# Performance work log

Measured on AMD Instinct MI355X. Metric: run time of the kernel, lower is better.

Reference implementation:

```python
import jax, jax.numpy as jnp
import numpy as np

N = 1024      # n_nodes
S = 32        # state_dim
M = 32        # message_dim
STEPS = 5     # n_steps


def setup_inputs() -> dict:
    key = jax.random.key(0)
    ks = jax.random.split(key, 12)
    w = lambda k, shape: jax.random.normal(k, shape, jnp.float32) * 0.02
    return {
        "J": jax.random.normal(ks[0], (N, N), jnp.float32),
        "b": jax.random.normal(ks[1], (N,), jnp.float32),
        # message_passing MLP (Linear(2S+3->M), Linear(M->M), Linear(M->M))
        "W1": w(ks[2], (M, 2 * S + 3)), "b1": jnp.zeros((M,), jnp.float32),
        "W2": w(ks[3], (M, M)),         "b2": jnp.zeros((M,), jnp.float32),
        "W3": w(ks[4], (M, M)),         "b3": jnp.zeros((M,), jnp.float32),
        # GRU(input=S+M, hidden=S). h0 is always zero in the original forward,
        # so weight_hh never contributes (only bias_hh does) and is omitted.
        "W_ih": w(ks[5], (3 * S, S + M)),
        "b_ih": w(ks[6], (3 * S,)),
        "b_hh": w(ks[7], (3 * S,)),
        # readout MLP (Linear(S->M), Linear(M->M), Linear(M->2))
        "R1": w(ks[8], (M, S)),  "rb1": jnp.zeros((M,), jnp.float32),
        "R2": w(ks[9], (M, M)),  "rb2": jnp.zeros((M,), jnp.float32),
        "R3": w(ks[10], (2, M)), "rb3": jnp.zeros((2,), jnp.float32),
    }


def reference(J, b, W1, b1, W2, b2, W3, b3, W_ih, b_ih, b_hh, R1, rb1, R2, rb2, R3, rb3):
    # Split first linear over the concat [h_i, h_j, J_ij, b_i, b_j] so the
    # [N, N, 2S+3] concat tensor is never materialized.
    W1a, W1b = W1[:, :S], W1[:, S:2 * S]
    wJ, wbi, wbj = W1[:, 2 * S], W1[:, 2 * S + 1], W1[:, 2 * S + 2]

    def step(h, _):
        hi = h @ W1a.T                       # [N, M] (sender part)
        hj = h @ W1b.T                       # [N, M] (receiver part)
        pre = (hi[:, None, :] + hj[None, :, :]
               + J[:, :, None] * wJ
               + b[:, None, None] * wbi
               + b[None, :, None] * wbj
               + b1)                          # [N, N, M]
        x = jax.nn.relu(pre)
        x = jax.nn.relu(x @ W2.T + b2)
        x = jax.nn.relu(x @ W3.T + b3)       # message_i_j: [N, N, M]
        m = x.sum(0)                          # message to node j: sum over senders i
        # GRU with zero initial hidden state: h' = (1-z) * n_gate
        gi = jnp.concatenate([h, m], axis=-1) @ W_ih.T + b_ih  # [N, 3S]
        r = jax.nn.sigmoid(gi[:, :S] + b_hh[:S])
        z = jax.nn.sigmoid(gi[:, S:2 * S] + b_hh[S:2 * S])
        n = jnp.tanh(gi[:, 2 * S:] + r * b_hh[2 * S:])
        return (1.0 - z) * n, None

    h0 = jnp.zeros((N, S), J.dtype)
    h, _ = jax.lax.scan(step, h0, None, length=STEPS)

    r = jax.nn.relu(h @ R1.T + rb1)
    r = jax.nn.relu(r @ R2.T + rb2)
    r = jax.nn.relu(r @ R3.T + rb3)          # [N, 2]
    return jax.nn.sigmoid(r)
```

## Files before the change

kernel.cpp:

```cpp
#include <hip/hip_runtime.h>
#include <math.h>

#define NN 1024

typedef __attribute__((ext_vector_type(8))) short bf16x8;
typedef __attribute__((ext_vector_type(4))) float f32x4;
typedef __attribute__((ext_vector_type(2))) float f32x2;
typedef __attribute__((ext_vector_type(4))) unsigned int u32x4;

__device__ __forceinline__ float sigmoidf_(float x) { return 1.0f / (1.0f + __expf(-x)); }

__device__ __forceinline__ unsigned int pk2(float a, float b) {
    return __builtin_amdgcn_perm(__float_as_uint(a) + 0x8000u,
                                 __float_as_uint(b) + 0x8000u, 0x03020706u);
}
__device__ __forceinline__ unsigned int pkcvt(float a, float b) {
#if __has_builtin(__builtin_amdgcn_cvt_pk_bf16_f32)
    return __builtin_bit_cast(unsigned int, __builtin_amdgcn_cvt_pk_bf16_f32(a, b));
#else
    return pk2(a, b);
#endif
}
__device__ __forceinline__ unsigned short f2bf_rne(float a) {
    unsigned int ua = __float_as_uint(a);
    ua += 0x7fffu + ((ua >> 16) & 1u);
    return (unsigned short)(ua >> 16);
}

#define CFG_FLOATS 2560

__global__ __launch_bounds__(256) void k_pre(
    const float* __restrict__ J, const float* __restrict__ b,
    const float* __restrict__ W1, const float* __restrict__ b1,
    const float* __restrict__ W2, const float* __restrict__ b2,
    const float* __restrict__ W3, const float* __restrict__ b3,
    float* __restrict__ Jt, float* __restrict__ h,
    float* __restrict__ u0, float* __restrict__ v, float* __restrict__ cfg)
{
    __shared__ float tile[32][33];
    const int t = blockIdx.x;
    const int tid = threadIdx.x;
    if (t < 1024) {
        int tx = (t & 31) * 32, ty = (t >> 5) * 32;
        int x = tid & 31, y = tid >> 5;
#pragma unroll
        for (int r = 0; r < 4; r++)
            tile[y + 8 * r][x] = J[(size_t)(ty + y + 8 * r) * NN + tx + x];
        __syncthreads();
#pragma unroll
        for (int r = 0; r < 4; r++)
            Jt[(size_t)(tx + y + 8 * r) * NN + ty + x] = tile[x][y + 8 * r];
    } else if (t < 1152) {
        int idx = (t - 1024) * 256 + tid;
        int row = idx >> 5, mm = idx & 31;
        float bi = b[row];
        h[idx]  = 0.f;
        u0[idx] = bi * W1[mm * 67 + 65];
        v[idx]  = fmaf(bi, W1[mm * 67 + 66], b1[mm]);
    } else if (tid < 64) {
        const int l = tid, p = l & 15, q = l >> 4;
        union FU { unsigned int d[4]; unsigned short s[8]; } t0, t1, t2, t3;
        float wj[8];
#pragma unroll
        for (int jj = 0; jj < 8; jj++) {
            int k = q * 8 + jj;
            t0.s[jj] = f2bf_rne(W2[p * 32 + k]);
            t1.s[jj] = f2bf_rne(W2[(16 + p) * 32 + k]);
            t2.s[jj] = f2bf_rne(W3[p * 32 + k]);
            t3.s[jj] = f2bf_rne(W3[(16 + p) * 32 + k]);
            wj[jj] = W1[k * 67 + 64];
        }
        u32x4* cw = (u32x4*)cfg;
        cw[l]       = *(u32x4*)t0.d;
        cw[64 + l]  = *(u32x4*)t1.d;
        cw[128 + l] = *(u32x4*)t2.d;
        cw[192 + l] = *(u32x4*)t3.d;
        f32x4* cf = (f32x4*)(cfg + 1024);
        f32x4 v0, v1, v2, v3;
#pragma unroll
        for (int r = 0; r < 4; r++) {
            v0[r] = b2[q * 4 + r];  v1[r] = b2[16 + q * 4 + r];
            v2[r] = b3[q * 4 + r];  v3[r] = b3[16 + q * 4 + r];
        }
        cf[l] = v0; cf[64 + l] = v1; cf[128 + l] = v2; cf[192 + l] = v3;
        f32x4* cj = (f32x4*)(cfg + 2048);
        f32x4 wlo, whi;
#pragma unroll
        for (int r = 0; r < 4; r++) { wlo[r] = wj[r]; whi[r] = wj[4 + r]; }
        cj[l] = wlo; cj[64 + l] = whi;
    }
}

__device__ __forceinline__ void tile_body(
    float jw, const float4& ua_c, const float4& ub_c,
    const f32x2* vv2, const f32x2* wj2,
    const bf16x8& w2a0, const bf16x8& w2a1,
    const bf16x8& w3a0, const bf16x8& w3a1,
    const f32x4& b2v0, const f32x4& b2v1,
    const f32x4& b3v0, const f32x4& b3v1,
    int s0, int s1, bool qlo, f32x4& acc0, f32x4& acc1)
{
    const f32x2 jw2 = {jw, jw};
    const f32x2 z2 = {0.f, 0.f};
    const f32x4 z4 = {0.f, 0.f, 0.f, 0.f};

    f32x2 x0 = {ua_c.x, ua_c.y}, x1 = {ua_c.z, ua_c.w};
    f32x2 x2 = {ub_c.x, ub_c.y}, x3 = {ub_c.z, ub_c.w};
    x0 = jw2 * wj2[0] + (x0 + vv2[0]);
    x1 = jw2 * wj2[1] + (x1 + vv2[1]);
    x2 = jw2 * wj2[2] + (x2 + vv2[2]);
    x3 = jw2 * wj2[3] + (x3 + vv2[3]);
    x0 = __builtin_elementwise_max(x0, z2);
    x1 = __builtin_elementwise_max(x1, z2);
    x2 = __builtin_elementwise_max(x2, z2);
    x3 = __builtin_elementwise_max(x3, z2);

    union BU { u32x4 u4; bf16x8 v; unsigned int d[4]; } bx;
    bx.d[0] = pkcvt(x0[0], x0[1]);
    bx.d[1] = pkcvt(x1[0], x1[1]);
    bx.d[2] = pkcvt(x2[0], x2[1]);
    bx.d[3] = pkcvt(x3[0], x3[1]);

    f32x4 c0 = __builtin_amdgcn_mfma_f32_16x16x32_bf16(w2a0, bx.v, b2v0, 0, 0, 0);
    f32x4 c1 = __builtin_amdgcn_mfma_f32_16x16x32_bf16(w2a1, bx.v, b2v1, 0, 0, 0);
    c0 = __builtin_elementwise_max(c0, z4);
    c1 = __builtin_elementwise_max(c1, z4);

    const int d0 = (int)pkcvt(c0[0], c0[1]);
    const int d1 = (int)pkcvt(c0[2], c0[3]);
    const int d2 = (int)pkcvt(c1[0], c1[1]);
    const int d3 = (int)pkcvt(c1[2], c1[3]);

    const int A0 = __builtin_amdgcn_ds_bpermute(s0, d0);
    const int A1 = __builtin_amdgcn_ds_bpermute(s0, d1);
    const int A2 = __builtin_amdgcn_ds_bpermute(s1, d0);
    const int A3 = __builtin_amdgcn_ds_bpermute(s1, d1);
    const int B0 = __builtin_amdgcn_ds_bpermute(s0, d2);
    const int B1 = __builtin_amdgcn_ds_bpermute(s0, d3);
    const int B2 = __builtin_amdgcn_ds_bpermute(s1, d2);
    const int B3 = __builtin_amdgcn_ds_bpermute(s1, d3);

    union BU yr;
    yr.d[0] = (unsigned)(qlo ? A0 : B0);
    yr.d[1] = (unsigned)(qlo ? A1 : B1);
    yr.d[2] = (unsigned)(qlo ? A2 : B2);
    yr.d[3] = (unsigned)(qlo ? A3 : B3);

    f32x4 e0 = __builtin_amdgcn_mfma_f32_16x16x32_bf16(w3a0, yr.v, b3v0, 0, 0, 0);
    f32x4 e1 = __builtin_amdgcn_mfma_f32_16x16x32_bf16(w3a1, yr.v, b3v1, 0, 0, 0);
    acc0 = acc0 + __builtin_elementwise_max(e0, z4);
    acc1 = acc1 + __builtin_elementwise_max(e1, z4);
}

__global__ __launch_bounds__(256, 4) void k_step(
    const float* __restrict__ Jt, const float* __restrict__ cfg,
    const float* __restrict__ Wih, const float* __restrict__ bih,
    const float* __restrict__ bhh, const float* __restrict__ b,
    const float* __restrict__ b1, const float* __restrict__ W1,
    const float* __restrict__ R1, const float* __restrict__ rb1,
    const float* __restrict__ R2, const float* __restrict__ rb2,
    const float* __restrict__ R3, const float* __restrict__ rb3,
    float* __restrict__ h, float* __restrict__ v,
    const float* __restrict__ ui, float* __restrict__ uo,
    float* __restrict__ out, int do_out)
{
    __shared__ float red[4 * 32];
    __shared__ float hm[64], gbuf[96], hnb[32], tb[32];

    const int tid = threadIdx.x;
    const int w = tid >> 6;
    const int l = tid & 63;
    const int p = l & 15;
    const int q = l >> 4;
    const int j = blockIdx.x;

    union FU { bf16x8 v; u32x4 u4; } w2a0, w2a1, w3a0, w3a1;
    const u32x4* cw = (const u32x4*)cfg;
    w2a0.u4 = cw[l]; w2a1.u4 = cw[64 + l]; w3a0.u4 = cw[128 + l]; w3a1.u4 = cw[192 + l];
    const f32x4* cf = (const f32x4*)(cfg + 1024);
    const f32x4 b2v0 = cf[l], b2v1 = cf[64 + l], b3v0 = cf[128 + l], b3v1 = cf[192 + l];
    const f32x4* cj = (const f32x4*)(cfg + 2048);
    const f32x4 wlo = cj[l], whi = cj[64 + l];
    f32x2 wj2[4] = { {wlo[0], wlo[1]}, {wlo[2], wlo[3]}, {whi[0], whi[1]}, {whi[2], whi[3]} };

    f32x2 vv2[4];
    {
        float4 va = *(const float4*)(v + j * 32 + q * 8);
        float4 vb = *(const float4*)(v + j * 32 + q * 8 + 4);
        vv2[0] = f32x2{va.x, va.y}; vv2[1] = f32x2{va.z, va.w};
        vv2[2] = f32x2{vb.x, vb.y}; vv2[3] = f32x2{vb.z, vb.w};
    }

    const int s0 = (p | ((l & 16) << 1)) << 2;
    const int s1 = s0 + 64;
    const bool qlo = (l & 32) == 0;

    f32x4 acc0 = {0.f, 0.f, 0.f, 0.f}, acc1 = {0.f, 0.f, 0.f, 0.f};

    const int ibase = w * 256;
    const float* jp = Jt + (size_t)j * NN + ibase + p;
    const float* up = ui + (size_t)(ibase + p) * 32 + q * 8;

    float  jwA = jp[0],  jwB = jp[16];
    float4 uaA = *(const float4*)(up);
    float4 ubA = *(const float4*)(up + 4);
    float4 uaB = *(const float4*)(up + 512);
    float4 ubB = *(const float4*)(up + 516);

#pragma unroll
    for (int tt = 0; tt < 8; ++tt) {
        const float  jwA_c = jwA; const float4 uaA_c = uaA, ubA_c = ubA;
        const float  jwB_c = jwB; const float4 uaB_c = uaB, ubB_c = ubB;
        if (tt < 7) {
            const float* jn = jp + (tt + 1) * 32;
            const float* un = up + (size_t)(tt + 1) * 1024;
            jwA = jn[0];  jwB = jn[16];
            uaA = *(const float4*)(un);
            ubA = *(const float4*)(un + 4);
            uaB = *(const float4*)(un + 512);
            ubB = *(const float4*)(un + 516);
        }
        tile_body(jwA_c, uaA_c, ubA_c, vv2, wj2, w2a0.v, w2a1.v, w3a0.v, w3a1.v,
                  b2v0, b2v1, b3v0, b3v1, s0, s1, qlo, acc0, acc1);
        tile_body(jwB_c, uaB_c, ubB_c, vv2, wj2, w2a0.v, w2a1.v, w3a0.v, w3a1.v,
                  b2v0, b2v1, b3v0, b3v1, s0, s1, qlo, acc0, acc1);
    }

#pragma unroll
    for (int bit = 1; bit < 16; bit <<= 1) {
#pragma unroll
        for (int r = 0; r < 4; r++) {
            acc0[r] += __shfl_xor(acc0[r], bit);
            acc1[r] += __shfl_xor(acc1[r], bit);
        }
    }
    if (p == 0) {
#pragma unroll
        for (int r = 0; r < 4; r++) {
            red[w * 32 + q * 4 + r]      = acc0[r];
            red[w * 32 + 16 + q * 4 + r] = acc1[r];
        }
    }
    __syncthreads();

    if (tid < 64) {
        float val;
        if (tid < 32) val = h[j * 32 + tid];
        else {
            int s = tid - 32;
            val = red[s] + red[32 + s] + red[64 + s] + red[96 + s];
        }
        hm[tid] = val;
    }
    __syncthreads();

    if (tid < 192) {
        const int row = tid >> 1, half = tid & 1;
        const float* wr = Wih + row * 64 + half * 32;
        const float* hh = hm + half * 32;
        float acc = 0.f;
#pragma unroll
        for (int k4 = 0; k4 < 8; k4++) {
            float4 w4 = *(const float4*)(wr + 4 * k4);
            acc = fmaf(w4.x, hh[4 * k4 + 0], acc);
            acc = fmaf(w4.y, hh[4 * k4 + 1], acc);
            acc = fmaf(w4.z, hh[4 * k4 + 2], acc);
            acc = fmaf(w4.w, hh[4 * k4 + 3], acc);
        }
        acc += __shfl_xor(acc, 1);
        if (half == 0) gbuf[row] = acc + bih[row];
    }
    __syncthreads();

    if (tid < 32) {
        const int s = tid;
        float r = sigmoidf_(gbuf[s] + bhh[s]);
        float z = sigmoidf_(gbuf[32 + s] + bhh[32 + s]);
        float n = tanhf(gbuf[64 + s] + r * bhh[64 + s]);
        float hn_ = (1.0f - z) * n;
        hnb[s] = hn_;
        h[j * 32 + s] = hn_;
    }
    __syncthreads();

    if (tid < 64) {
        const int s = tid & 31;
        const bool isV = tid >= 32;
        const float bj = b[j];
        const float* wr = W1 + s * 67 + (isV ? 32 : 0);
        float acc = isV ? fmaf(bj, W1[s * 67 + 66], b1[s]) : bj * W1[s * 67 + 65];
#pragma unroll
        for (int k = 0; k < 32; k++) acc = fmaf(wr[k], hnb[k], acc);
        if (isV) v[j * 32 + s] = acc;
        else     uo[j * 32 + s] = acc;
    }

    if (do_out) {
        __syncthreads();
        if (tid < 32) {
            float a = rb1[tid];
            const float* rr = R1 + tid * 32;
#pragma unroll 8
            for (int k = 0; k < 32; k++) a = fmaf(rr[k], hnb[k], a);
            gbuf[tid] = fmaxf(a, 0.f);
        }
        __syncthreads();
        if (tid < 32) {
            float a = rb2[tid];
            const float* rr = R2 + tid * 32;
#pragma unroll 8
            for (int k = 0; k < 32; k++) a = fmaf(rr[k], gbuf[k], a);
            tb[tid] = fmaxf(a, 0.f);
        }
        __syncthreads();
        if (tid < 2) {
            float a = rb3[tid];
            const float* rr = R3 + tid * 32;
#pragma unroll 8
            for (int k = 0; k < 32; k++) a = fmaf(rr[k], tb[k], a);
            out[j * 2 + tid] = sigmoidf_(fmaxf(a, 0.f));
        }
    }
}

extern "C" void kernel_launch(void* const* d_in, const int* in_sizes, int n_in,
                              void* d_out, int out_size, void* d_ws, size_t ws_size,
                              hipStream_t stream)
{
    const float* J   = (const float*)d_in[0];
    const float* b   = (const float*)d_in[1];
    const float* W1  = (const float*)d_in[2];
    const float* b1  = (const float*)d_in[3];
    const float* W2  = (const float*)d_in[4];
    const float* b2  = (const float*)d_in[5];
    const float* W3  = (const float*)d_in[6];
    const float* b3  = (const float*)d_in[7];
    const float* Wih = (const float*)d_in[8];
    const float* bih = (const float*)d_in[9];
    const float* bhh = (const float*)d_in[10];
    const float* R1  = (const float*)d_in[11];
    const float* rb1 = (const float*)d_in[12];
    const float* R2  = (const float*)d_in[13];
    const float* rb2 = (const float*)d_in[14];
    const float* R3  = (const float*)d_in[15];
    const float* rb3 = (const float*)d_in[16];

    float* out = (float*)d_out;
    float* ws  = (float*)d_ws;
    float* h   = ws;
    float* v   = ws + 32768;
    float* u0  = ws + 65536;
    float* u1  = ws + 98304;
    float* Jt  = ws + 131072;
    float* cfg = ws + 131072 + NN * NN;

    k_pre<<<1153, 256, 0, stream>>>(J, b, W1, b1, W2, b2, W3, b3,
                                    Jt, h, u0, v, cfg);
    for (int s = 0; s < 5; s++) {
        const float* ui = (s & 1) ? u1 : u0;
        float*       uo = (s & 1) ? u0 : u1;
        k_step<<<1024, 256, 0, stream>>>(Jt, cfg, Wih, bih, bhh, b, b1, W1,
                                         R1, rb1, R2, rb2, R3, rb3,
                                         h, v, ui, uo, out, (s == 4) ? 1 : 0);
    }
}
```

Baseline: 202.0 us.

## Replace bpermute transpose with K=16 MFMA chain for third MLP layer

The third message-MLP layer is restructured to use two chained 16x16x16 bf16 MFMAs whose operand layout matches the second layer's output registers directly. This removes the eight ds_bpermute cross-lane shuffles per tile and simplifies the final reduction to summing accumulator components plus two shuffles. W3 is prepacked in a new transposed layout in the preprocessing kernel. The operand prefetch is also deepened to two stages. The trade-off is twice as many (smaller) MFMA issues for layer three and more registers held for prefetched data.

```diff
diff --git a/kernel.cpp b/kernel.cpp
--- a/kernel.cpp
+++ b/kernel.cpp
@@ -4,9 +4,17 @@
 #define NN 1024
 
 typedef __attribute__((ext_vector_type(8))) short bf16x8;
+typedef __attribute__((ext_vector_type(4))) short bf16x4;
 typedef __attribute__((ext_vector_type(4))) float f32x4;
 typedef __attribute__((ext_vector_type(2))) float f32x2;
 typedef __attribute__((ext_vector_type(4))) unsigned int u32x4;
+
+#if __has_builtin(__builtin_amdgcn_mfma_f32_16x16x16bf16_1k)
+#define HAVE_MFMA16 1
+#define MFMA16(a, b, c) __builtin_amdgcn_mfma_f32_16x16x16bf16_1k((a), (b), (c), 0, 0, 0)
+#else
+#define HAVE_MFMA16 0
+#endif
 
 __device__ __forceinline__ float sigmoidf_(float x) { return 1.0f / (1.0f + __expf(-x)); }
 
@@ -26,8 +34,11 @@
     ua += 0x7fffu + ((ua >> 16) & 1u);
     return (unsigned short)(ua >> 16);
 }
-
-#define CFG_FLOATS 2560
+__device__ __forceinline__ unsigned int pk2b(float a, float b) {
+    return (unsigned int)f2bf_rne(a) | ((unsigned int)f2bf_rne(b) << 16);
+}
+
+#define CFG_FLOATS 3584
 
 __global__ __launch_bounds__(256) void k_pre(
     const float* __restrict__ J, const float* __restrict__ b,
@@ -88,68 +99,25 @@
 #pragma unroll
         for (int r = 0; r < 4; r++) { wlo[r] = wj[r]; whi[r] = wj[4 + r]; }
         cj[l] = wlo; cj[64 + l] = whi;
-    }
-}
-
-__device__ __forceinline__ void tile_body(
-    float jw, const float4& ua_c, const float4& ub_c,
-    const f32x2* vv2, const f32x2* wj2,
-    const bf16x8& w2a0, const bf16x8& w2a1,
-    const bf16x8& w3a0, const bf16x8& w3a1,
-    const f32x4& b2v0, const f32x4& b2v1,
-    const f32x4& b3v0, const f32x4& b3v1,
-    int s0, int s1, bool qlo, f32x4& acc0, f32x4& acc1)
-{
-    const f32x2 jw2 = {jw, jw};
-    const f32x2 z2 = {0.f, 0.f};
-    const f32x4 z4 = {0.f, 0.f, 0.f, 0.f};
-
-    f32x2 x0 = {ua_c.x, ua_c.y}, x1 = {ua_c.z, ua_c.w};
-    f32x2 x2 = {ub_c.x, ub_c.y}, x3 = {ub_c.z, ub_c.w};
-    x0 = jw2 * wj2[0] + (x0 + vv2[0]);
-    x1 = jw2 * wj2[1] + (x1 + vv2[1]);
-    x2 = jw2 * wj2[2] + (x2 + vv2[2]);
-    x3 = jw2 * wj2[3] + (x3 + vv2[3]);
-    x0 = __builtin_elementwise_max(x0, z2);
-    x1 = __builtin_elementwise_max(x1, z2);
-    x2 = __builtin_elementwise_max(x2, z2);
-    x3 = __builtin_elementwise_max(x3, z2);
-
-    union BU { u32x4 u4; bf16x8 v; unsigned int d[4]; } bx;
-    bx.d[0] = pkcvt(x0[0], x0[1]);
-    bx.d[1] = pkcvt(x1[0], x1[1]);
-    bx.d[2] = pkcvt(x2[0], x2[1]);
-    bx.d[3] = pkcvt(x3[0], x3[1]);
-
-    f32x4 c0 = __builtin_amdgcn_mfma_f32_16x16x32_bf16(w2a0, bx.v, b2v0, 0, 0, 0);
-    f32x4 c1 = __builtin_amdgcn_mfma_f32_16x16x32_bf16(w2a1, bx.v, b2v1, 0, 0, 0);
-    c0 = __builtin_elementwise_max(c0, z4);
-    c1 = __builtin_elementwise_max(c1, z4);
-
-    const int d0 = (int)pkcvt(c0[0], c0[1]);
-    const int d1 = (int)pkcvt(c0[2], c0[3]);
-    const int d2 = (int)pkcvt(c1[0], c1[1]);
-    const int d3 = (int)pkcvt(c1[2], c1[3]);
-
-    const int A0 = __builtin_amdgcn_ds_bpermute(s0, d0);
-    const int A1 = __builtin_amdgcn_ds_bpermute(s0, d1);
-    const int A2 = __builtin_amdgcn_ds_bpermute(s1, d0);
-    const int A3 = __builtin_amdgcn_ds_bpermute(s1, d1);
-    const int B0 = __builtin_amdgcn_ds_bpermute(s0, d2);
-    const int B1 = __builtin_amdgcn_ds_bpermute(s0, d3);
-    const int B2 = __builtin_amdgcn_ds_bpermute(s1, d2);
-    const int B3 = __builtin_amdgcn_ds_bpermute(s1, d3);
-
-    union BU yr;
-    yr.d[0] = (unsigned)(qlo ? A0 : B0);
-    yr.d[1] = (unsigned)(qlo ? A1 : B1);
-    yr.d[2] = (unsigned)(qlo ? A2 : B2);
-    yr.d[3] = (unsigned)(qlo ? A3 : B3);
-
-    f32x4 e0 = __builtin_amdgcn_mfma_f32_16x16x32_bf16(w3a0, yr.v, b3v0, 0, 0, 0);
-    f32x4 e1 = __builtin_amdgcn_mfma_f32_16x16x32_bf16(w3a1, yr.v, b3v1, 0, 0, 0);
-    acc0 = acc0 + __builtin_elementwise_max(e0, z4);
-    acc1 = acc1 + __builtin_elementwise_max(e1, z4);
+
+        const int g = p;
+        u32x4 fa, fb;
+        fa[0] = pk2b(W3[g * 32 + 4 * q + 0],      W3[g * 32 + 4 * q + 1]);
+        fa[1] = pk2b(W3[g * 32 + 4 * q + 2],      W3[g * 32 + 4 * q + 3]);
+        fa[2] = pk2b(W3[g * 32 + 16 + 4 * q + 0], W3[g * 32 + 16 + 4 * q + 1]);
+        fa[3] = pk2b(W3[g * 32 + 16 + 4 * q + 2], W3[g * 32 + 16 + 4 * q + 3]);
+        fb[0] = pk2b(W3[(16 + g) * 32 + 4 * q + 0],      W3[(16 + g) * 32 + 4 * q + 1]);
+        fb[1] = pk2b(W3[(16 + g) * 32 + 4 * q + 2],      W3[(16 + g) * 32 + 4 * q + 3]);
+        fb[2] = pk2b(W3[(16 + g) * 32 + 16 + 4 * q + 0], W3[(16 + g) * 32 + 16 + 4 * q + 1]);
+        fb[3] = pk2b(W3[(16 + g) * 32 + 16 + 4 * q + 2], W3[(16 + g) * 32 + 16 + 4 * q + 3]);
+        u32x4* cw2 = (u32x4*)(cfg + 2560);
+        cw2[l] = fa; cw2[64 + l] = fb;
+        f32x4* cb3 = (f32x4*)(cfg + 3072);
+        f32x4 r0, r1;
+#pragma unroll
+        for (int r = 0; r < 4; r++) { r0[r] = b3[g]; r1[r] = b3[16 + g]; }
+        cb3[l] = r0; cb3[64 + l] = r1;
+    }
 }
 
 __global__ __launch_bounds__(256, 4) void k_step(
@@ -174,14 +142,33 @@
     const int q = l >> 4;
     const int j = blockIdx.x;
 
-    union FU { bf16x8 v; u32x4 u4; } w2a0, w2a1, w3a0, w3a1;
+    union FU { bf16x8 v; u32x4 u4; } w2a0, w2a1;
     const u32x4* cw = (const u32x4*)cfg;
-    w2a0.u4 = cw[l]; w2a1.u4 = cw[64 + l]; w3a0.u4 = cw[128 + l]; w3a1.u4 = cw[192 + l];
+    w2a0.u4 = cw[l]; w2a1.u4 = cw[64 + l];
     const f32x4* cf = (const f32x4*)(cfg + 1024);
-    const f32x4 b2v0 = cf[l], b2v1 = cf[64 + l], b3v0 = cf[128 + l], b3v1 = cf[192 + l];
+    const f32x4 b2v0 = cf[l], b2v1 = cf[64 + l];
     const f32x4* cj = (const f32x4*)(cfg + 2048);
     const f32x4 wlo = cj[l], whi = cj[64 + l];
     f32x2 wj2[4] = { {wlo[0], wlo[1]}, {wlo[2], wlo[3]}, {whi[0], whi[1]}, {whi[2], whi[3]} };
+
+#if HAVE_MFMA16
+    union B4 { bf16x4 v; unsigned int d[2]; } B0a, B1a, B0b, B1b;
+    {
+        const u32x4* cw2 = (const u32x4*)(cfg + 2560);
+        u32x4 fa = cw2[l], fb = cw2[64 + l];
+        B0a.d[0] = fa[0]; B0a.d[1] = fa[1]; B1a.d[0] = fa[2]; B1a.d[1] = fa[3];
+        B0b.d[0] = fb[0]; B0b.d[1] = fb[1]; B1b.d[0] = fb[2]; B1b.d[1] = fb[3];
+    }
+    const f32x4* cb3 = (const f32x4*)(cfg + 3072);
+    const f32x4 b3lo = cb3[l], b3hi = cb3[64 + l];
+#else
+    union FU w3a0, w3a1;
+    w3a0.u4 = cw[128 + l]; w3a1.u4 = cw[192 + l];
+    const f32x4 b3v0 = cf[128 + l], b3v1 = cf[192 + l];
+    const int s0 = (p | ((l & 16) << 1)) << 2;
+    const int s1 = s0 + 64;
+    const bool qlo = (l & 32) == 0;
+#endif
 
     f32x2 vv2[4];
     {
@@ -191,41 +178,115 @@
         vv2[2] = f32x2{vb.x, vb.y}; vv2[3] = f32x2{vb.z, vb.w};
     }
 
-    const int s0 = (p | ((l & 16) << 1)) << 2;
-    const int s1 = s0 + 64;
-    const bool qlo = (l & 32) == 0;
-
     f32x4 acc0 = {0.f, 0.f, 0.f, 0.f}, acc1 = {0.f, 0.f, 0.f, 0.f};
 
     const int ibase = w * 256;
     const float* jp = Jt + (size_t)j * NN + ibase + p;
     const float* up = ui + (size_t)(ibase + p) * 32 + q * 8;
 
-    float  jwA = jp[0],  jwB = jp[16];
-    float4 uaA = *(const float4*)(up);
-    float4 ubA = *(const float4*)(up + 4);
-    float4 uaB = *(const float4*)(up + 512);
-    float4 ubB = *(const float4*)(up + 516);
+    float  jw0[2], jw1[2];
+    float4 ua0[2], ub0[2], ua1[2], ub1[2];
+#pragma unroll
+    for (int s = 0; s < 2; s++) {
+        jw0[s] = jp[s * 32];       jw1[s] = jp[s * 32 + 16];
+        ua0[s] = *(const float4*)(up + (size_t)s * 1024);
+        ub0[s] = *(const float4*)(up + (size_t)s * 1024 + 4);
+        ua1[s] = *(const float4*)(up + (size_t)s * 1024 + 512);
+        ub1[s] = *(const float4*)(up + (size_t)s * 1024 + 516);
+    }
 
 #pragma unroll
     for (int tt = 0; tt < 8; ++tt) {
-        const float  jwA_c = jwA; const float4 uaA_c = uaA, ubA_c = ubA;
-        const float  jwB_c = jwB; const float4 uaB_c = uaB, ubB_c = ubB;
-        if (tt < 7) {
-            const float* jn = jp + (tt + 1) * 32;
-            const float* un = up + (size_t)(tt + 1) * 1024;
-            jwA = jn[0];  jwB = jn[16];
-            uaA = *(const float4*)(un);
-            ubA = *(const float4*)(un + 4);
-            uaB = *(const float4*)(un + 512);
-            ubB = *(const float4*)(un + 516);
-        }
-        tile_body(jwA_c, uaA_c, ubA_c, vv2, wj2, w2a0.v, w2a1.v, w3a0.v, w3a1.v,
-                  b2v0, b2v1, b3v0, b3v1, s0, s1, qlo, acc0, acc1);
-        tile_body(jwB_c, uaB_c, ubB_c, vv2, wj2, w2a0.v, w2a1.v, w3a0.v, w3a1.v,
-                  b2v0, b2v1, b3v0, b3v1, s0, s1, qlo, acc0, acc1);
-    }
-
+        const int sl = tt & 1;
+        const float  jwA_c = jw0[sl], jwB_c = jw1[sl];
+        const float4 uaA_c = ua0[sl], ubA_c = ub0[sl];
+        const float4 uaB_c = ua1[sl], ubB_c = ub1[sl];
+        if (tt < 6) {
+            const float* jn = jp + (tt + 2) * 32;
+            const float* un = up + (size_t)(tt + 2) * 1024;
+            jw0[sl] = jn[0];  jw1[sl] = jn[16];
+            ua0[sl] = *(const float4*)(un);
+            ub0[sl] = *(const float4*)(un + 4);
+            ua1[sl] = *(const float4*)(un + 512);
+            ub1[sl] = *(const float4*)(un + 516);
+        }
+
+#pragma unroll
+        for (int half = 0; half < 2; ++half) {
+            const float  jw = half ? jwB_c : jwA_c;
+            const float4 ua_c = half ? uaB_c : uaA_c;
+            const float4 ub_c = half ? ubB_c : ubA_c;
+
+            const f32x2 jw2 = {jw, jw};
+            const f32x2 z2 = {0.f, 0.f};
+            const f32x4 z4 = {0.f, 0.f, 0.f, 0.f};
+
+            f32x2 x0 = {ua_c.x, ua_c.y}, x1 = {ua_c.z, ua_c.w};
+            f32x2 x2 = {ub_c.x, ub_c.y}, x3 = {ub_c.z, ub_c.w};
+            x0 = jw2 * wj2[0] + (x0 + vv2[0]);
+            x1 = jw2 * wj2[1] + (x1 + vv2[1]);
+            x2 = jw2 * wj2[2] + (x2 + vv2[2]);
+            x3 = jw2 * wj2[3] + (x3 + vv2[3]);
+            x0 = __builtin_elementwise_max(x0, z2);
+            x1 = __builtin_elementwise_max(x1, z2);
+            x2 = __builtin_elementwise_max(x2, z2);
+            x3 = __builtin_elementwise_max(x3, z2);
+
+            union BU { u32x4 u4; bf16x8 v; unsigned int d[4]; } bx;
+            bx.d[0] = pkcvt(x0[0], x0[1]);
+            bx.d[1] = pkcvt(x1[0], x1[1]);
+            bx.d[2] = pkcvt(x2[0], x2[1]);
+            bx.d[3] = pkcvt(x3[0], x3[1]);
+
+            f32x4 c0 = __builtin_amdgcn_mfma_f32_16x16x32_bf16(w2a0.v, bx.v, b2v0, 0, 0, 0);
+            f32x4 c1 = __builtin_amdgcn_mfma_f32_16x16x32_bf16(w2a1.v, bx.v, b2v1, 0, 0, 0);
+            c0 = __builtin_elementwise_max(c0, z4);
+            c1 = __builtin_elementwise_max(c1, z4);
+
+#if HAVE_MFMA16
+            union B4 { bf16x4 v; unsigned int d[2]; } A0, A1;
+            A0.d[0] = pkcvt(c0[0], c0[1]); A0.d[1] = pkcvt(c0[2], c0[3]);
+            A1.d[0] = pkcvt(c1[0], c1[1]); A1.d[1] = pkcvt(c1[2], c1[3]);
+
+            f32x4 e0 = MFMA16(A0.v, B0a.v, b3lo);
+            e0 = MFMA16(A1.v, B1a.v, e0);
+            f32x4 e1 = MFMA16(A0.v, B0b.v, b3hi);
+            e1 = MFMA16(A1.v, B1b.v, e1);
+            acc0 = acc0 + __builtin_elementwise_max(e0, z4);
+            acc1 = acc1 + __builtin_elementwise_max(e1, z4);
+#else
+            const int d0 = (int)pkcvt(c0[0], c0[1]);
+            const int d1 = (int)pkcvt(c0[2], c0[3]);
+            const int d2 = (int)pkcvt(c1[0], c1[1]);
+            const int d3 = (int)pkcvt(c1[2], c1[3]);
+            const int A0_ = __builtin_amdgcn_ds_bpermute(s0, d0);
+            const int A1_ = __builtin_amdgcn_ds_bpermute(s0, d1);
+            const int A2_ = __builtin_amdgcn_ds_bpermute(s1, d0);
+            const int A3_ = __builtin_amdgcn_ds_bpermute(s1, d1);
+            const int B0_ = __builtin_amdgcn_ds_bpermute(s0, d2);
+            const int B1_ = __builtin_amdgcn_ds_bpermute(s0, d3);
+            const int B2_ = __builtin_amdgcn_ds_bpermute(s1, d2);
+            const int B3_ = __builtin_amdgcn_ds_bpermute(s1, d3);
+            union BU yr;
+            yr.d[0] = (unsigned)(qlo ? A0_ : B0_);
+            yr.d[1] = (unsigned)(qlo ? A1_ : B1_);
+            yr.d[2] = (unsigned)(qlo ? A2_ : B2_);
+            yr.d[3] = (unsigned)(qlo ? A3_ : B3_);
+            f32x4 e0 = __builtin_amdgcn_mfma_f32_16x16x32_bf16(w3a0.v, yr.v, b3v0, 0, 0, 0);
+            f32x4 e1 = __builtin_amdgcn_mfma_f32_16x16x32_bf16(w3a1.v, yr.v, b3v1, 0, 0, 0);
+            acc0 = acc0 + __builtin_elementwise_max(e0, z4);
+            acc1 = acc1 + __builtin_elementwise_max(e1, z4);
+#endif
+        }
+    }
+
+#if HAVE_MFMA16
+    float s0v = acc0[0] + acc0[1] + acc0[2] + acc0[3];
+    float s1v = acc1[0] + acc1[1] + acc1[2] + acc1[3];
+    s0v += __shfl_xor(s0v, 16);  s0v += __shfl_xor(s0v, 32);
+    s1v += __shfl_xor(s1v, 16);  s1v += __shfl_xor(s1v, 32);
+    if (l < 16) { red[w * 32 + l] = s0v;  red[w * 32 + 16 + l] = s1v; }
+#else
 #pragma unroll
     for (int bit = 1; bit < 16; bit <<= 1) {
 #pragma unroll
@@ -241,6 +302,7 @@
             red[w * 32 + 16 + q * 4 + r] = acc1[r];
         }
     }
+#endif
     __syncthreads();
 
     if (tid < 64) {
```

New measurement: 200.9 us, median of 2. No clear change (-0.5%).
